# Kernel optimization log

Measured on AMD Instinct MI355X. Metric: run time of the kernel, lower is better.

The kernel has to match this reference:

```python
import jax, jax.numpy as jnp
import numpy as np

N, CAMS = 1, 4
C1, C2, NH = 256, 256, 8
H1, H2, W2 = 128, 64, 400
H, W = 128, 128


def setup_inputs() -> dict:
    key = jax.random.key(0)
    ks = jax.random.split(key, 16)
    sc = 0.02
    th = jax.random.uniform(ks[3], (N, CAMS)) * 2.0 * np.pi
    c, s = jnp.cos(th), jnp.sin(th)
    z, o = jnp.zeros_like(c), jnp.ones_like(c)
    rots = jnp.stack([jnp.stack([c, -s, z], -1), jnp.stack([s, c, z], -1), jnp.stack([z, z, o], -1)], -2)
    return {
        "list_a": jax.random.normal(ks[0], (N, C1, H, W), jnp.float32),
        "list_b": jax.random.normal(ks[1], (N * CAMS, C2, H2, W2), jnp.float32),
        "fov_list": jax.random.uniform(ks[2], (N, CAMS)) * 0.5 + 1.0,
        "rots_list": rots.astype(jnp.float32),
        "trans_list": jax.random.normal(ks[4], (N, CAMS, 3), jnp.float32),
        "fxs": jax.random.uniform(ks[5], (N, CAMS)) * 100.0 + 500.0,
        "cxs": jax.random.uniform(ks[6], (N, CAMS)) * 20.0 + 390.0,
        "pos_a": jax.random.normal(ks[7], (1, H1, C1), jnp.float32),
        "pos_b": jax.random.normal(ks[8], (1, H2, C2), jnp.float32),
        "Wq": jax.random.normal(ks[9], (C1, C1), jnp.float32) * sc,
        "bq": jnp.zeros((C1,), jnp.float32),
        "Wk": jax.random.normal(ks[10], (C1, C2), jnp.float32) * sc,
        "bk": jnp.zeros((C1,), jnp.float32),
        "Wv": jax.random.normal(ks[11], (C1, C2), jnp.float32) * sc,
        "bv": jnp.zeros((C1,), jnp.float32),
        "in_w": jax.random.normal(ks[12], (3 * C1, C1), jnp.float32) * sc,
        "in_b": jnp.zeros((3 * C1,), jnp.float32),
        "out_w": jax.random.normal(ks[13], (C1, C1), jnp.float32) * sc,
        "out_b": jnp.zeros((C1,), jnp.float32),
    }


def _polar_coords(w1, h1, Hh, Ww, rots, fx, cx):
    # per-pixel viewing angles from intrinsics (original image width hard-coded 800)
    pi = jnp.arange(w1, dtype=jnp.float32)
    pw = 800.0 / w1
    ang = jnp.arctan((pi * pw + pw / 2.0 - cx) / fx)
    R90 = jnp.array([[0.0, 1.0], [-1.0, 0.0]], jnp.float32)
    rot = R90 @ rots[:2, :2].astype(jnp.float32)
    cr, sr = rot[0, 0], rot[1, 0]
    ca = cr * jnp.cos(ang) + sr * jnp.sin(ang)
    sa = -sr * jnp.cos(ang) + cr * jnp.sin(ang)
    cxp = jnp.float32(Ww // 2)
    cyp = jnp.float32(Hh // 2)
    rmax = jnp.sqrt(cxp ** 2 + cyp ** 2)
    radii = jnp.linspace(0.0, 1.0, h1).reshape(h1, 1) * rmax
    x = cxp + radii * ca  # [h1, w1]
    y = cyp - radii * sa
    return x, y


def _bilinear(img, x, y):
    # img [C,H,W]; x,y pixel coords [h1,w1]; grid_sample(align_corners=True) after clamping
    Hh, Ww = img.shape[1], img.shape[2]
    x = jnp.clip(x, 0.0, Ww - 1.0)
    y = jnp.clip(y, 0.0, Hh - 1.0)
    x0 = jnp.floor(x); y0 = jnp.floor(y)
    x1 = jnp.clip(x0 + 1.0, 0.0, Ww - 1.0)
    y1 = jnp.clip(y0 + 1.0, 0.0, Hh - 1.0)
    wx = x - x0; wy = y - y0
    x0i, x1i = x0.astype(jnp.int32), x1.astype(jnp.int32)
    y0i, y1i = y0.astype(jnp.int32), y1.astype(jnp.int32)
    v00 = img[:, y0i, x0i]; v01 = img[:, y0i, x1i]
    v10 = img[:, y1i, x0i]; v11 = img[:, y1i, x1i]
    return v00 * (1 - wx) * (1 - wy) + v01 * wx * (1 - wy) + v10 * (1 - wx) * wy + v11 * wx * wy


def _mha(q, k, v, in_w, in_b, out_w, out_b, nh):
    E = q.shape[-1]
    dh = E // nh
    qq = q @ in_w[:E].T + in_b[:E]
    kk = k @ in_w[E:2 * E].T + in_b[E:2 * E]
    vv = v @ in_w[2 * E:].T + in_b[2 * E:]
    B, Lq, _ = q.shape
    Lk = k.shape[1]
    qq = qq.reshape(B, Lq, nh, dh)
    kk = kk.reshape(B, Lk, nh, dh)
    vv = vv.reshape(B, Lk, nh, dh)
    att = jnp.einsum('bqhd,bkhd->bhqk', qq, kk) / jnp.sqrt(jnp.float32(dh))
    p = jax.nn.softmax(att, axis=-1)
    o = jnp.einsum('bhqk,bkhd->bqhd', p, vv).reshape(B, Lq, E)
    return o @ out_w.T + out_b


def _forward(list_a, list_b, rots_list, fxs, cxs, pos_a, pos_b,
             Wq, bq, Wk, bk, Wv, bv, in_w, in_b, out_w, out_b):
    outs = []
    for i in range(list_a.shape[0]):
        a = list_a[i]
        C1_, h1, Wb = a.shape
        Hb = h1
        enh = None
        for j in (0, 3):  # cameras 1 and 2 are skipped by the original `continue`
            b = list_b[i * CAMS + j]
            C2_, h2, w2 = b.shape
            x, y = _polar_coords(w2, h1, a.shape[1], a.shape[2], rots_list[i, j], fxs[i, j], cxs[i, j])
            a_rect = _bilinear(a, x, y)                     # [C1, h1, w2]
            a_seq = jnp.transpose(a_rect, (2, 1, 0)) + pos_a  # [w2, h1, C1]
            b_seq = jnp.transpose(b, (2, 1, 0)) + pos_b       # [w2, h2, C2]
            q = a_seq @ Wq.T + bq
            k = b_seq @ Wk.T + bk
            v = b_seq @ Wv.T + bv
            o = _mha(q, k, v, in_w, in_b, out_w, out_b, NH)
            a_enh = jnp.transpose(o, (2, 1, 0))              # [C1, h1, w2]
            # scatter-add restore with nearest-pixel indices
            xi = jnp.clip(jnp.round(x), 0, a.shape[2] - 1).astype(jnp.int32)
            yi = jnp.clip(jnp.round(y), 0, a.shape[1] - 1).astype(jnp.int32)
            idx = (yi * a.shape[2] + xi).reshape(-1)
            vals = a_enh.reshape(C1_, -1)
            rest = jnp.zeros((C1_, a.shape[1] * a.shape[2]), a.dtype).at[:, idx].add(vals)
            cnt = jnp.zeros((a.shape[1] * a.shape[2],), a.dtype).at[idx].add(1.0)
            cnt = jnp.where(cnt == 0, 1.0, cnt)
            enh = (rest / cnt).reshape(a.shape)
            a = a + enh
        outs.append(a + enh)  # original double-adds the last camera's enhancement
    return jnp.stack(outs)


def reference(list_a, list_b, fov_list, rots_list, trans_list, fxs, cxs, pos_a, pos_b,
              Wq, bq, Wk, bk, Wv, bv, in_w, in_b, out_w, out_b):
    # fov_list / trans_list are accepted but unused in the original math path
    return _forward(list_a, list_b, rots_list, fxs, cxs, pos_a, pos_b,
                    Wq, bq, Wk, bk, Wv, bv, in_w, in_b, out_w, out_b)
```

## Files before the change

### kernel.cpp

```cpp
#include <hip/hip_runtime.h>

#define PIX 16384
#define MS 51200
#define MB 25600

typedef __attribute__((ext_vector_type(8))) short short8;
typedef __attribute__((ext_vector_type(4))) float floatx4;

__device__ inline ushort f2b(float x) {
  uint u = __float_as_uint(x);
  return (ushort)((u + 0x7fffu + ((u >> 16) & 1u)) >> 16);
}
__device__ inline float b2f(ushort u) {
  return __uint_as_float(((uint)u) << 16);
}

__global__ __launch_bounds__(256) void coords_kernel(
    const float* __restrict__ rots, const float* __restrict__ fxs,
    const float* __restrict__ cxs,
    float* __restrict__ xarr, float* __restrict__ yarr,
    int* __restrict__ idxarr, float* __restrict__ cnt)
{
  int jz = blockIdx.y;
  int j = jz ? 3 : 0;
  int s = blockIdx.x * 256 + threadIdx.x;
  int h = s / 400;
  int w = s - h * 400;
  float fx = fxs[j], cx = cxs[j];
  const float* R = rots + j * 9;
  float cr = R[3];
  float sr = -R[0];
  float t = (2.0f * (float)w + 1.0f - cx) / fx;
  float inv = 1.0f / sqrtf(1.0f + t * t);
  float ca = (cr + sr * t) * inv;
  float sa = (cr * t - sr) * inv;
  float rad = ((float)h * (1.0f / 127.0f)) * 90.50966799187808f;
  float x = 64.0f + rad * ca;
  float y = 64.0f - rad * sa;
  xarr[jz * MS + s] = x;
  yarr[jz * MS + s] = y;
  int xi = (int)fminf(fmaxf(rintf(x), 0.0f), 127.0f);
  int yi = (int)fminf(fmaxf(rintf(y), 0.0f), 127.0f);
  int pix = yi * 128 + xi;
  idxarr[jz * MS + s] = pix;
  atomicAdd(&cnt[jz * PIX + pix], 1.0f);
}

__global__ __launch_bounds__(256) void prefix_kernel(
    const float* __restrict__ cntg, int* __restrict__ offsetsg)
{
  const float* cnt = cntg + blockIdx.x * PIX;
  int* offsets = offsetsg + blockIdx.x * PIX;
  __shared__ int sh[256];
  int t = threadIdx.x;
  int base = t * 64;
  const float4* cp = (const float4*)(cnt + base);
  int sum = 0;
#pragma unroll
  for (int i = 0; i < 16; ++i) {
    float4 v = cp[i];
    sum += (int)v.x + (int)v.y + (int)v.z + (int)v.w;
  }
  sh[t] = sum;
  __syncthreads();
  for (int d = 1; d < 256; d <<= 1) {
    int v = (t >= d) ? sh[t - d] : 0;
    __syncthreads();
    sh[t] += v;
    __syncthreads();
  }
  int run = sh[t] - sum;
  int4* op = (int4*)(offsets + base);
#pragma unroll
  for (int i = 0; i < 16; ++i) {
    float4 v = cp[i];
    int a0 = (int)v.x, a1 = (int)v.y, a2 = (int)v.z, a3 = (int)v.w;
    int4 o;
    o.x = run; o.y = run + a0; o.z = run + a0 + a1; o.w = run + a0 + a1 + a2;
    op[i] = o;
    run += a0 + a1 + a2 + a3;
  }
}

__global__ __launch_bounds__(256) void fill_kernel(
    const int* __restrict__ idxarr, const int* __restrict__ offsets,
    int* __restrict__ cursor, int* __restrict__ order, int* __restrict__ pixs)
{
  int jz = blockIdx.y;
  int s = blockIdx.x * 256 + threadIdx.x;
  int pix = idxarr[jz * MS + s];
  int pos = offsets[jz * PIX + pix] + atomicAdd(&cursor[jz * PIX + pix], 1);
  order[jz * MS + pos] = (s % 400) * 128 + (s / 400);
  pixs[jz * MS + pos] = pix;
}

__global__ __launch_bounds__(256) void transpose_kernel(
    const float* __restrict__ src, ushort* __restrict__ dst)
{
  __shared__ float tile[64][65];
  int p0 = blockIdx.x * 64;
  int c0 = blockIdx.y * 64;
  int t = threadIdx.x;
  int pr = (t & 15) * 4;
  int cr = t >> 4;
#pragma unroll
  for (int q = 0; q < 4; ++q) {
    int c = cr + q * 16;
    float4 v = *(const float4*)(src + (size_t)(c0 + c) * PIX + p0 + pr);
    tile[pr + 0][c] = v.x;
    tile[pr + 1][c] = v.y;
    tile[pr + 2][c] = v.z;
    tile[pr + 3][c] = v.w;
  }
  __syncthreads();
  int p = t >> 2;
  int ch = (t & 3) * 16;
  ushort tmp[16];
#pragma unroll
  for (int i = 0; i < 16; ++i) tmp[i] = f2b(tile[p][ch + i]);
  ushort* d = dst + (size_t)(p0 + p) * 256 + c0 + ch;
  *(uint4*)(d) = *(uint4*)tmp;
  *(uint4*)(d + 8) = *(uint4*)(tmp + 8);
}

__global__ __launch_bounds__(256) void misc_kernel(
    const float* __restrict__ out_w, ushort* __restrict__ out_wh,
    const float* __restrict__ in_w, const float* __restrict__ in_b,
    const float* __restrict__ bq, const float* __restrict__ bk,
    const float* __restrict__ bv, float* __restrict__ beff)
{
  if (blockIdx.x < 64) {
    int t = blockIdx.x * 256 + threadIdx.x;
    float4 v = ((const float4*)out_w)[t];
    ushort4 o;
    o.x = f2b(v.x); o.y = f2b(v.y); o.z = f2b(v.z); o.w = f2b(v.w);
    ((ushort4*)out_wh)[t] = o;
  } else {
    int z = blockIdx.x - 64;
    int f = threadIdx.x;
    const float* bsrc = (z == 0) ? bq : ((z == 1) ? bk : bv);
    const float* row = in_w + (size_t)(z * 256 + f) * 256;
    float acc = in_b[z * 256 + f];
    for (int e = 0; e < 256; ++e) acc += row[e] * bsrc[e];
    beff[z * 256 + f] = acc;
  }
}

#define LFP 264
__device__ __forceinline__ void sampleproj_body(
    ushort* lf, int bx,
    const ushort* __restrict__ aT, const float* __restrict__ xarr,
    const float* __restrict__ yarr, const ushort* __restrict__ Wh,
    const float* __restrict__ bias, ushort* __restrict__ qh)
{
  int s0 = bx * 64;
  int tid = threadIdx.x;
  int lane = tid & 63;
  int wave = tid >> 6;
  int col = lane & 15, quad = lane >> 4;
  int c0 = lane * 4;

#pragma unroll 4
  for (int i = 0; i < 16; ++i) {
    int sl = wave * 16 + i;
    int s = s0 + sl;
    float x = fminf(fmaxf(xarr[s], 0.0f), 127.0f);
    float y = fminf(fmaxf(yarr[s], 0.0f), 127.0f);
    float x0f = floorf(x), y0f = floorf(y);
    int x0 = (int)x0f, y0 = (int)y0f;
    int x1 = min(x0 + 1, 127), y1 = min(y0 + 1, 127);
    float wx = x - x0f, wy = y - y0f;
    float w00 = (1.0f - wx) * (1.0f - wy);
    float w01 = wx * (1.0f - wy);
    float w10 = (1.0f - wx) * wy;
    float w11 = wx * wy;
    ushort4 v00 = *(const ushort4*)(aT + (size_t)(y0 * 128 + x0) * 256 + c0);
    ushort4 v01 = *(const ushort4*)(aT + (size_t)(y0 * 128 + x1) * 256 + c0);
    ushort4 v10 = *(const ushort4*)(aT + (size_t)(y1 * 128 + x0) * 256 + c0);
    ushort4 v11 = *(const ushort4*)(aT + (size_t)(y1 * 128 + x1) * 256 + c0);
    ushort4 o;
    o.x = f2b(w00 * b2f(v00.x) + w01 * b2f(v01.x) + w10 * b2f(v10.x) + w11 * b2f(v11.x));
    o.y = f2b(w00 * b2f(v00.y) + w01 * b2f(v01.y) + w10 * b2f(v10.y) + w11 * b2f(v11.y));
    o.z = f2b(w00 * b2f(v00.z) + w01 * b2f(v01.z) + w10 * b2f(v10.z) + w11 * b2f(v11.z));
    o.w = f2b(w00 * b2f(v00.w) + w01 * b2f(v01.w) + w10 * b2f(v10.w) + w11 * b2f(v11.w));
    *(ushort4*)&lf[sl * LFP + c0] = o;
  }
  __syncthreads();

  int fw = wave * 64;
  floatx4 acc[4][4];
#pragma unroll
  for (int i = 0; i < 4; ++i)
#pragma unroll
    for (int jx = 0; jx < 4; ++jx) acc[i][jx] = (floatx4){0.f, 0.f, 0.f, 0.f};

  for (int kb = 0; kb < 256; kb += 32) {
    short8 aop[4], bop[4];
#pragma unroll
    for (int tf = 0; tf < 4; ++tf)
      aop[tf] = *(const short8*)(Wh + (size_t)(fw + tf * 16 + col) * 256 + kb + quad * 8);
#pragma unroll
    for (int ts = 0; ts < 4; ++ts)
      bop[ts] = *(const short8*)&lf[(ts * 16 + col) * LFP + kb + quad * 8];
#pragma unroll
    for (int ts = 0; ts < 4; ++ts)
#pragma unroll
      for (int tf = 0; tf < 4; ++tf)
        acc[ts][tf] = __builtin_amdgcn_mfma_f32_16x16x32_bf16(
            aop[tf], bop[ts], acc[ts][tf], 0, 0, 0);
  }
#pragma unroll
  for (int ts = 0; ts < 4; ++ts) {
    int s = s0 + ts * 16 + col;
    int h = s / 400;
    size_t obase = (size_t)s * 256;
#pragma unroll
    for (int tf = 0; tf < 4; ++tf) {
      int f = fw + tf * 16 + quad * 4;
      float4 bv = *(const float4*)(bias + h * 256 + f);
      ushort4 ov;
      ov.x = f2b(acc[ts][tf][0] + bv.x);
      ov.y = f2b(acc[ts][tf][1] + bv.y);
      ov.z = f2b(acc[ts][tf][2] + bv.z);
      ov.w = f2b(acc[ts][tf][3] + bv.w);
      *(ushort4*)(qh + obase + f) = ov;
    }
  }
}

__device__ __forceinline__ void projKV_body(
    ushort* lb, int bx,
    const float* __restrict__ bsrc,
    const ushort* __restrict__ WhK, const ushort* __restrict__ WhV,
    const float* __restrict__ biasK, const float* __restrict__ biasV,
    ushort* __restrict__ kh, ushort* __restrict__ vh)
{
  int m0 = bx * 64;
  int tid = threadIdx.x;
  int lane = tid & 63;
  int wave = tid >> 6;
  int col = lane & 15, quad = lane >> 4;
  int fw = wave * 64;

  int m4 = (tid & 15) * 4;
  int c4 = (tid >> 4) * 4;
#pragma unroll
  for (int cq = 0; cq < 4; ++cq) {
    int c = c4 + cq * 64;
    float4 v0 = *(const float4*)(bsrc + (size_t)(c + 0) * MB + m0 + m4);
    float4 v1 = *(const float4*)(bsrc + (size_t)(c + 1) * MB + m0 + m4);
    float4 v2 = *(const float4*)(bsrc + (size_t)(c + 2) * MB + m0 + m4);
    float4 v3 = *(const float4*)(bsrc + (size_t)(c + 3) * MB + m0 + m4);
    ushort4 w0; w0.x = f2b(v0.x); w0.y = f2b(v1.x); w0.z = f2b(v2.x); w0.w = f2b(v3.x);
    ushort4 w1; w1.x = f2b(v0.y); w1.y = f2b(v1.y); w1.z = f2b(v2.y); w1.w = f2b(v3.y);
    ushort4 w2; w2.x = f2b(v0.z); w2.y = f2b(v1.z); w2.z = f2b(v2.z); w2.w = f2b(v3.z);
    ushort4 w3; w3.x = f2b(v0.w); w3.y = f2b(v1.w); w3.z = f2b(v2.w); w3.w = f2b(v3.w);
    *(ushort4*)&lb[(m4 + 0) * LFP + c] = w0;
    *(ushort4*)&lb[(m4 + 1) * LFP + c] = w1;
    *(ushort4*)&lb[(m4 + 2) * LFP + c] = w2;
    *(ushort4*)&lb[(m4 + 3) * LFP + c] = w3;
  }
  __syncthreads();

  for (int z = 0; z < 2; ++z) {
    const ushort* Wh = z ? WhV : WhK;
    const float* bias = z ? biasV : biasK;
    ushort* out = z ? vh : kh;
    floatx4 acc[4][4];
#pragma unroll
    for (int i = 0; i < 4; ++i)
#pragma unroll
      for (int jx = 0; jx < 4; ++jx) acc[i][jx] = (floatx4){0.f, 0.f, 0.f, 0.f};

    for (int kb = 0; kb < 256; kb += 32) {
      short8 bop[4], aop[4];
#pragma unroll
      for (int ts = 0; ts < 4; ++ts)
        bop[ts] = *(const short8*)&lb[(ts * 16 + col) * LFP + kb + quad * 8];
#pragma unroll
      for (int tf = 0; tf < 4; ++tf)
        aop[tf] = *(const short8*)(Wh + (size_t)(fw + tf * 16 + col) * 256 + kb + quad * 8);
#pragma unroll
      for (int ts = 0; ts < 4; ++ts)
#pragma unroll
        for (int tf = 0; tf < 4; ++tf)
          acc[ts][tf] = __builtin_amdgcn_mfma_f32_16x16x32_bf16(
              aop[tf], bop[ts], acc[ts][tf], 0, 0, 0);
    }
#pragma unroll
    for (int ts = 0; ts < 4; ++ts) {
      int m = m0 + ts * 16 + col;
      int h = m / 400;
      size_t obase = (size_t)m * 256;
#pragma unroll
      for (int tf = 0; tf < 4; ++tf) {
        int f = fw + tf * 16 + quad * 4;
        float4 bv = *(const float4*)(bias + h * 256 + f);
        ushort4 ov;
        ov.x = f2b(acc[ts][tf][0] + bv.x);
        ov.y = f2b(acc[ts][tf][1] + bv.y);
        ov.z = f2b(acc[ts][tf][2] + bv.z);
        ov.w = f2b(acc[ts][tf][3] + bv.w);
        *(ushort4*)(out + obase + f) = ov;
      }
    }
  }
}

__global__ __launch_bounds__(256, 3) void proj_kernel(
    const ushort* __restrict__ aT, const float* __restrict__ xarr,
    const float* __restrict__ yarr, const ushort* __restrict__ weffh,
    const float* __restrict__ qpos, ushort* __restrict__ qh,
    const float* __restrict__ bsrc,
    const float* __restrict__ kpos, const float* __restrict__ vpos,
    ushort* __restrict__ kh, ushort* __restrict__ vh)
{
  __shared__ ushort lf[64 * LFP];
  if (blockIdx.x < 400)
    projKV_body(lf, blockIdx.x, bsrc, weffh + 65536, weffh + 131072,
                kpos, vpos, kh, vh);
  else
    sampleproj_body(lf, blockIdx.x - 400, aT, xarr, yarr, weffh, qpos, qh);
}

#define VP 72
#define PP 72
__global__ __launch_bounds__(256) void attn_mfma_kernel(
    const ushort* __restrict__ qh, const ushort* __restrict__ kh,
    const ushort* __restrict__ vh, ushort* __restrict__ obuf)
{
  __shared__ ushort lV[4][32 * VP];
  __shared__ ushort lP[4][16 * PP];
  int b = blockIdx.x;
  int hg = blockIdx.y & 1;
  int qb = blockIdx.y >> 1;
  int wave = threadIdx.x >> 6;
  int lane = threadIdx.x & 63;
  int head = hg * 4 + wave;
  int col = lane & 15, quad = lane >> 4;
  ushort* Vw = lV[wave];
  ushort* Pw = lP[wave];

  short8 bk0 = *(const short8*)(kh + ((size_t)(( 0 + col) * 400 + b)) * 256 + head * 32 + quad * 8);
  short8 bk1 = *(const short8*)(kh + ((size_t)((16 + col) * 400 + b)) * 256 + head * 32 + quad * 8);
  short8 bk2 = *(const short8*)(kh + ((size_t)((32 + col) * 400 + b)) * 256 + head * 32 + quad * 8);
  short8 bk3 = *(const short8*)(kh + ((size_t)((48 + col) * 400 + b)) * 256 + head * 32 + quad * 8);

  {
    const ushort* vsrc = vh + ((size_t)(lane * 400 + b)) * 256 + head * 32;
    ushort vr[32];
    *(uint4*)(vr) = *(const uint4*)(vsrc);
    *(uint4*)(vr + 8) = *(const uint4*)(vsrc + 8);
    *(uint4*)(vr + 16) = *(const uint4*)(vsrc + 16);
    *(uint4*)(vr + 24) = *(const uint4*)(vsrc + 24);
#pragma unroll
    for (int d = 0; d < 32; ++d) Vw[d * VP + lane] = vr[d];
  }
  short8 vA0 = *(const short8*)(Vw + (col) * VP + 0 * 32 + quad * 8);
  short8 vB0 = *(const short8*)(Vw + (16 + col) * VP + 0 * 32 + quad * 8);
  short8 vA1 = *(const short8*)(Vw + (col) * VP + 1 * 32 + quad * 8);
  short8 vB1 = *(const short8*)(Vw + (16 + col) * VP + 1 * 32 + quad * 8);

  const float scl = 0.17677669529663687f;
  for (int qt = qb * 4; qt < qb * 4 + 4; ++qt) {
    short8 aq = *(const short8*)(qh +
        ((size_t)((qt * 16 + col) * 400 + b)) * 256 + head * 32 + quad * 8);
    floatx4 s0 = {0.f,0.f,0.f,0.f}, s1 = s0, s2 = s0, s3 = s0;
    s0 = __builtin_amdgcn_mfma_f32_16x16x32_bf16(aq, bk0, s0, 0, 0, 0);
    s1 = __builtin_amdgcn_mfma_f32_16x16x32_bf16(aq, bk1, s1, 0, 0, 0);
    s2 = __builtin_amdgcn_mfma_f32_16x16x32_bf16(aq, bk2, s2, 0, 0, 0);
    s3 = __builtin_amdgcn_mfma_f32_16x16x32_bf16(aq, bk3, s3, 0, 0, 0);
    float e[4][4], mr[4], sm[4];
#pragma unroll
    for (int r = 0; r < 4; ++r) {
      float v0 = s0[r] * scl, v1 = s1[r] * scl;
      float v2 = s2[r] * scl, v3 = s3[r] * scl;
      e[0][r] = v0; e[1][r] = v1; e[2][r] = v2; e[3][r] = v3;
      mr[r] = fmaxf(fmaxf(v0, v1), fmaxf(v2, v3));
    }
#pragma unroll
    for (int mask = 1; mask <= 8; mask <<= 1)
#pragma unroll
      for (int r = 0; r < 4; ++r)
        mr[r] = fmaxf(mr[r], __shfl_xor(mr[r], mask, 64));
#pragma unroll
    for (int r = 0; r < 4; ++r) {
      float acc = 0.f;
#pragma unroll
      for (int t = 0; t < 4; ++t) {
        float ev = __expf(e[t][r] - mr[r]);
        e[t][r] = ev;
        acc += ev;
      }
      sm[r] = acc;
    }
#pragma unroll
    for (int mask = 1; mask <= 8; mask <<= 1)
#pragma unroll
      for (int r = 0; r < 4; ++r)
        sm[r] += __shfl_xor(sm[r], mask, 64);
#pragma unroll
    for (int t = 0; t < 4; ++t)
#pragma unroll
      for (int r = 0; r < 4; ++r)
        Pw[(quad * 4 + r) * PP + t * 16 + col] = f2b(e[t][r]);
    floatx4 o0 = {0.f,0.f,0.f,0.f}, o1 = o0;
    {
      short8 ap0 = *(const short8*)(Pw + col * PP + 0 * 32 + quad * 8);
      o0 = __builtin_amdgcn_mfma_f32_16x16x32_bf16(ap0, vA0, o0, 0, 0, 0);
      o1 = __builtin_amdgcn_mfma_f32_16x16x32_bf16(ap0, vB0, o1, 0, 0, 0);
      short8 ap1 = *(const short8*)(Pw + col * PP + 1 * 32 + quad * 8);
      o0 = __builtin_amdgcn_mfma_f32_16x16x32_bf16(ap1, vA1, o0, 0, 0, 0);
      o1 = __builtin_amdgcn_mfma_f32_16x16x32_bf16(ap1, vB1, o1, 0, 0, 0);
    }
#pragma unroll
    for (int r = 0; r < 4; ++r) {
      float iv = 1.0f / sm[r];
      Pw[(quad * 4 + r) * PP + col] = f2b(o0[r] * iv);
      Pw[(quad * 4 + r) * PP + 16 + col] = f2b(o1[r] * iv);
    }
    int orow = lane >> 2, ochunk = lane & 3;
    uint4 ov = *(const uint4*)(Pw + orow * PP + ochunk * 8);
    *(uint4*)(obuf + (size_t)(b * 128 + qt * 16 + orow) * 256 + head * 32 + ochunk * 8) = ov;
  }
}

__global__ __launch_bounds__(256) void gemmN3_kernel(
    const float* __restrict__ pos_a, const float* __restrict__ pos_b,
    const float* __restrict__ weff, const float* __restrict__ beff,
    float* __restrict__ qpos, float* __restrict__ kpos, float* __restrict__ vpos)
{
  int z = blockIdx.z;
  if (z > 0 && blockIdx.x > 0) return;
  const float* A = (z == 0) ? pos_a : pos_b;
  const float* Wt = weff + (size_t)z * 65536;
  const float* biasf = beff + z * 256;
  float* Cout = (z == 0) ? qpos : ((z == 1) ? kpos : vpos);
  __shared__ float As[64][17];
  __shared__ float Ws[16][65];
  int m0 = blockIdx.x * 64;
  int n0 = blockIdx.y * 64;
  int tid = threadIdx.x;
  int tx = tid & 15, ty = tid >> 4;
  float acc[4][4] = {};
  for (int k0 = 0; k0 < 256; k0 += 16) {
    {
      int m = tid >> 2;
      int kq = (tid & 3) << 2;
      float4 v = *(const float4*)(A + (size_t)(m0 + m) * 256 + k0 + kq);
      As[m][kq + 0] = v.x; As[m][kq + 1] = v.y;
      As[m][kq + 2] = v.z; As[m][kq + 3] = v.w;
    }
    {
      int f = tid >> 2;
      int kq = (tid & 3) << 2;
      float4 v = *(const float4*)(Wt + (size_t)(n0 + f) * 256 + k0 + kq);
      Ws[kq + 0][f] = v.x; Ws[kq + 1][f] = v.y;
      Ws[kq + 2][f] = v.z; Ws[kq + 3][f] = v.w;
    }
    __syncthreads();
#pragma unroll
    for (int kk = 0; kk < 16; ++kk) {
      float a[4], b[4];
#pragma unroll
      for (int i = 0; i < 4; ++i) a[i] = As[ty * 4 + i][kk];
#pragma unroll
      for (int jj = 0; jj < 4; ++jj) b[jj] = Ws[kk][tx * 4 + jj];
#pragma unroll
      for (int i = 0; i < 4; ++i)
#pragma unroll
        for (int jj = 0; jj < 4; ++jj) acc[i][jj] += a[i] * b[jj];
    }
    __syncthreads();
  }
#pragma unroll
  for (int i = 0; i < 4; ++i) {
    int m = m0 + ty * 4 + i;
    int f = n0 + tx * 4;
    float4 bv = *(const float4*)(biasf + f);
    float4 ov;
    ov.x = acc[i][0] + bv.x; ov.y = acc[i][1] + bv.y;
    ov.z = acc[i][2] + bv.z; ov.w = acc[i][3] + bv.w;
    *(float4*)(Cout + (size_t)m * 256 + f) = ov;
  }
}

__global__ __launch_bounds__(256) void gemm_ab_kernel(
    const float* __restrict__ in_w, const float* __restrict__ Wq,
    const float* __restrict__ Wk, const float* __restrict__ Wv,
    float* __restrict__ weff, ushort* __restrict__ weffh)
{
  int z = blockIdx.z;
  const float* A = in_w + (size_t)z * 65536;
  const float* B = (z == 0) ? Wq : ((z == 1) ? Wk : Wv);
  float* C = weff + (size_t)z * 65536;
  ushort* Ch = weffh + (size_t)z * 65536;
  __shared__ float As[64][17];
  __shared__ float Bs[16][64];
  int m0 = blockIdx.x * 64;
  int n0 = blockIdx.y * 64;
  int tid = threadIdx.x;
  int tx = tid & 15, ty = tid >> 4;
  float acc[4][4] = {};
  for (int k0 = 0; k0 < 256; k0 += 16) {
    {
      int m = tid >> 2;
      int kq = (tid & 3) << 2;
      float4 v = *(const float4*)(A + (size_t)(m0 + m) * 256 + k0 + kq);
      As[m][kq + 0] = v.x; As[m][kq + 1] = v.y;
      As[m][kq + 2] = v.z; As[m][kq + 3] = v.w;
    }
    {
      int k = tid >> 4;
      int nq = (tid & 15) << 2;
      float4 v = *(const float4*)(B + (size_t)(k0 + k) * 256 + n0 + nq);
      *(float4*)(&Bs[k][nq]) = v;
    }
    __syncthreads();
#pragma unroll
    for (int kk = 0; kk < 16; ++kk) {
      float a[4], b[4];
#pragma unroll
      for (int i = 0; i < 4; ++i) a[i] = As[ty * 4 + i][kk];
#pragma unroll
      for (int jj = 0; jj < 4; ++jj) b[jj] = Bs[kk][tx * 4 + jj];
#pragma unroll
      for (int i = 0; i < 4; ++i)
#pragma unroll
        for (int jj = 0; jj < 4; ++jj) acc[i][jj] += a[i] * b[jj];
    }
    __syncthreads();
  }
#pragma unroll
  for (int i = 0; i < 4; ++i) {
    int m = m0 + ty * 4 + i;
    *(float4*)(C + (size_t)m * 256 + n0 + tx * 4) = *(float4*)&acc[i][0];
    ushort4 hv;
    hv.x = f2b(acc[i][0]); hv.y = f2b(acc[i][1]);
    hv.z = f2b(acc[i][2]); hv.w = f2b(acc[i][3]);
    *(ushort4*)(Ch + (size_t)m * 256 + n0 + tx * 4) = hv;
  }
}

#define CH 64
__global__ __launch_bounds__(256) void segred_kernel(
    const ushort* __restrict__ obuf, const int* __restrict__ order,
    const int* __restrict__ pixs, float* __restrict__ osum)
{
  __shared__ int lm[CH];
  __shared__ int lp[CH + 2];
  int s0 = blockIdx.x * CH;
  int t = threadIdx.x;
  if (t < CH) {
    lm[t] = order[s0 + t];
    lp[t + 1] = pixs[s0 + t];
  } else if (t == CH) {
    lp[0] = (s0 > 0) ? pixs[s0 - 1] : -1;
  } else if (t == CH + 1) {
    lp[CH + 1] = (s0 + CH < MS) ? pixs[s0 + CH] : -2;
  }
  __syncthreads();
  int c = t;
  float va[8];
#pragma unroll
  for (int k = 0; k < 8; ++k)
    va[k] = b2f(obuf[(size_t)lm[k] * 256 + c]);
  float acc = 0.0f;
  int runBegin = 0;
#pragma unroll
  for (int i = 0; i < CH; ++i) {
    float v = va[i & 7];
    if (i + 8 < CH) va[i & 7] = b2f(obuf[(size_t)lm[i + 8] * 256 + c]);
    acc += v;
    int p = lp[i + 1];
    bool last = (i == CH - 1);
    if (last || p != lp[i + 2]) {
      bool pBeg = (runBegin == 0) && (p == lp[0]);
      bool pEnd = last && (p == lp[CH + 1]);
      float* dst = osum + (size_t)p * 256 + c;
      if (pBeg || pEnd) atomicAdd(dst, acc);
      else *dst = acc;
      acc = 0.0f;
      runBegin = i + 1;
    }
  }
}

__global__ __launch_bounds__(256) void outproj_update_kernel(
    const float* __restrict__ osum, const ushort* __restrict__ out_wh,
    const float* __restrict__ asrc, float* __restrict__ adst,
    const float* __restrict__ cnt, const float* __restrict__ out_b,
    float scale, ushort* __restrict__ aTout, int writeAT)
{
  int p0 = blockIdx.x * 32;
  int lane = threadIdx.x & 63;
  int wave = threadIdx.x >> 6;
  int col = lane & 15, quad = lane >> 4;
  int fw = wave * 64;
  floatx4 acc[2][4];
#pragma unroll
  for (int i = 0; i < 2; ++i)
#pragma unroll
    for (int jx = 0; jx < 4; ++jx) acc[i][jx] = (floatx4){0.f, 0.f, 0.f, 0.f};

  for (int kb = 0; kb < 256; kb += 32) {
    short8 aop[4], bop[2];
#pragma unroll
    for (int tf = 0; tf < 4; ++tf)
      aop[tf] = *(const short8*)(out_wh +
          (size_t)(fw + tf * 16 + col) * 256 + kb + quad * 8);
#pragma unroll
    for (int ts = 0; ts < 2; ++ts) {
      const float* brow = osum + (size_t)(p0 + ts * 16 + col) * 256 + kb + quad * 8;
      float4 f0 = *(const float4*)brow;
      float4 f1 = *(const float4*)(brow + 4);
      short8 bv;
      bv[0] = (short)f2b(f0.x); bv[1] = (short)f2b(f0.y);
      bv[2] = (short)f2b(f0.z); bv[3] = (short)f2b(f0.w);
      bv[4] = (short)f2b(f1.x); bv[5] = (short)f2b(f1.y);
      bv[6] = (short)f2b(f1.z); bv[7] = (short)f2b(f1.w);
      bop[ts] = bv;
    }
#pragma unroll
    for (int ts = 0; ts < 2; ++ts)
#pragma unroll
      for (int tf = 0; tf < 4; ++tf)
        acc[ts][tf] = __builtin_amdgcn_mfma_f32_16x16x32_bf16(
            aop[tf], bop[ts], acc[ts][tf], 0, 0, 0);
  }
#pragma unroll
  for (int ts = 0; ts < 2; ++ts) {
    int p = p0 + ts * 16 + col;
    float cn = cnt[p];
    float rs = scale / fmaxf(cn, 1.0f);
#pragma unroll
    for (int tf = 0; tf < 4; ++tf) {
      int f = fw + tf * 16 + quad * 4;
      float4 ob = *(const float4*)(out_b + f);
      float r0 = asrc[(size_t)(f + 0) * PIX + p] + (acc[ts][tf][0] + cn * ob.x) * rs;
      float r1 = asrc[(size_t)(f + 1) * PIX + p] + (acc[ts][tf][1] + cn * ob.y) * rs;
      float r2 = asrc[(size_t)(f + 2) * PIX + p] + (acc[ts][tf][2] + cn * ob.z) * rs;
      float r3 = asrc[(size_t)(f + 3) * PIX + p] + (acc[ts][tf][3] + cn * ob.w) * rs;
      adst[(size_t)(f + 0) * PIX + p] = r0;
      adst[(size_t)(f + 1) * PIX + p] = r1;
      adst[(size_t)(f + 2) * PIX + p] = r2;
      adst[(size_t)(f + 3) * PIX + p] = r3;
      if (writeAT) {
        ushort4 hv;
        hv.x = f2b(r0); hv.y = f2b(r1); hv.z = f2b(r2); hv.w = f2b(r3);
        *(ushort4*)(aTout + (size_t)p * 256 + f) = hv;
      }
    }
  }
}

extern "C" void kernel_launch(void* const* d_in, const int* in_sizes, int n_in,
                              void* d_out, int out_size, void* d_ws, size_t ws_size,
                              hipStream_t stream) {
  const float* list_a = (const float*)d_in[0];
  const float* list_b = (const float*)d_in[1];
  const float* rots   = (const float*)d_in[3];
  const float* fxs    = (const float*)d_in[5];
  const float* cxs    = (const float*)d_in[6];
  const float* pos_a  = (const float*)d_in[7];
  const float* pos_b  = (const float*)d_in[8];
  const float* Wq     = (const float*)d_in[9];
  const float* bq     = (const float*)d_in[10];
  const float* Wk     = (const float*)d_in[11];
  const float* bk     = (const float*)d_in[12];
  const float* Wv     = (const float*)d_in[13];
  const float* bv     = (const float*)d_in[14];
  const float* in_w   = (const float*)d_in[15];
  const float* in_b   = (const float*)d_in[16];
  const float* out_w  = (const float*)d_in[17];
  const float* out_b  = (const float*)d_in[18];

  float* ws      = (float*)d_ws;
  float* weff    = ws;
  float* beff    = weff + 196608;
  float* qpos    = beff + 768;
  float* kpos    = qpos + 32768;
  float* vpos    = kpos + 16384;
  float* a_cur   = vpos + 16384;
  float* xarr    = a_cur + 4194304;
  float* yarr    = xarr + 102400;
  int*   idxarr  = (int*)(yarr + 102400);
  int*   offs    = idxarr + 102400;
  int*   order   = offs + 32768;
  int*   pixs    = order + 102400;
  float* cnt     = (float*)(pixs + 102400);
  int*   cursor  = (int*)(cnt + 32768);
  float* osum    = (float*)(cursor + 32768);
  ushort* weffh  = (ushort*)(osum + 4194304);
  ushort* out_wh = weffh + 196608;
  ushort* obufh  = out_wh + 65536;
  ushort* qh     = obufh + 13107200;
  ushort* kh     = qh + 13107200;
  ushort* vh     = kh + 6553600;
  ushort* aT     = vh + 6553600;

  gemm_ab_kernel<<<dim3(4, 4, 3), 256, 0, stream>>>(in_w, Wq, Wk, Wv, weff, weffh);
  misc_kernel<<<67, 256, 0, stream>>>(out_w, out_wh, in_w, in_b, bq, bk, bv, beff);
  gemmN3_kernel<<<dim3(2, 4, 3), 256, 0, stream>>>(pos_a, pos_b, weff, beff,
                                                   qpos, kpos, vpos);
  hipMemsetAsync(cnt, 0, (size_t)(32768 + 32768) * sizeof(float), stream);
  coords_kernel<<<dim3(200, 2), 256, 0, stream>>>(rots, fxs, cxs, xarr, yarr, idxarr, cnt);
  prefix_kernel<<<2, 256, 0, stream>>>(cnt, offs);
  fill_kernel<<<dim3(200, 2), 256, 0, stream>>>(idxarr, offs, cursor, order, pixs);

  for (int jj = 0; jj < 2; ++jj) {
    int j = jj ? 3 : 0;
    const float* asrc = jj ? a_cur : list_a;
    hipMemsetAsync(osum, 0, (size_t)4194304 * sizeof(float), stream);
    if (jj == 0)
      transpose_kernel<<<dim3(256, 4), 256, 0, stream>>>(list_a, aT);
    proj_kernel<<<1200, 256, 0, stream>>>(aT, xarr + jj * MS, yarr + jj * MS,
                                          weffh, qpos, qh,
                                          list_b + (size_t)j * 6553600,
                                          kpos, vpos, kh, vh);
    attn_mfma_kernel<<<dim3(400, 4), 256, 0, stream>>>(qh, kh, vh, obufh);
    segred_kernel<<<800, 256, 0, stream>>>(obufh, order + jj * MS, pixs + jj * MS, osum);
    outproj_update_kernel<<<512, 256, 0, stream>>>(osum, out_wh, asrc,
                                                   jj ? (float*)d_out : a_cur,
                                                   cnt + jj * PIX, out_b,
                                                   jj ? 2.0f : 1.0f,
                                                   aT, jj == 0 ? 1 : 0);
  }
}
```

Measured before the change: 549.5 us.

## Fuse segmented reduction into out-projection kernel via CSR gather into LDS

Replaces the segment-reduce kernel, which wrote per-pixel sums to a global fp32 buffer with atomics, and the separate out-projection kernel with one kernel. The new kernel gathers each pixel's samples through the CSR offsets and counts, sums them into shared memory, and runs the MFMA out-projection from LDS. This drops the 16 MB osum memset, the global write and re-read of osum, and one launch per camera. The per-pixel gather loops vary in length, so work across waves may be uneven. Separately, proj_kernel's launch bounds move from 3 to 4 waves per EU, which may increase register pressure.

```diff
diff --git a/kernel.cpp b/kernel.cpp
--- a/kernel.cpp
+++ b/kernel.cpp
@@ -307,7 +307,7 @@
   }
 }
 
-__global__ __launch_bounds__(256, 3) void proj_kernel(
+__global__ __launch_bounds__(256, 4) void proj_kernel(
     const ushort* __restrict__ aT, const float* __restrict__ xarr,
     const float* __restrict__ yarr, const ushort* __restrict__ weffh,
     const float* __restrict__ qpos, ushort* __restrict__ qh,
@@ -542,59 +542,40 @@
   }
 }
 
-#define CH 64
-__global__ __launch_bounds__(256) void segred_kernel(
+#define OLF 260
+__global__ __launch_bounds__(256) void outred_kernel(
     const ushort* __restrict__ obuf, const int* __restrict__ order,
-    const int* __restrict__ pixs, float* __restrict__ osum)
-{
-  __shared__ int lm[CH];
-  __shared__ int lp[CH + 2];
-  int s0 = blockIdx.x * CH;
-  int t = threadIdx.x;
-  if (t < CH) {
-    lm[t] = order[s0 + t];
-    lp[t + 1] = pixs[s0 + t];
-  } else if (t == CH) {
-    lp[0] = (s0 > 0) ? pixs[s0 - 1] : -1;
-  } else if (t == CH + 1) {
-    lp[CH + 1] = (s0 + CH < MS) ? pixs[s0 + CH] : -2;
+    const int* __restrict__ offs, const float* __restrict__ cnt,
+    const ushort* __restrict__ out_wh,
+    const float* __restrict__ asrc, float* __restrict__ adst,
+    const float* __restrict__ out_b, float scale,
+    ushort* __restrict__ aTout, int writeAT)
+{
+  __shared__ float losum[32 * OLF];
+  int p0 = blockIdx.x * 32;
+  int tid = threadIdx.x;
+
+  {
+    int pg = tid >> 6;
+    int c0 = (tid & 63) * 4;
+    for (int pi = 0; pi < 8; ++pi) {
+      int p = p0 + pg * 8 + pi;
+      int beg = offs[p];
+      int num = (int)cnt[p];
+      float4 s4 = {0.f, 0.f, 0.f, 0.f};
+      for (int i = 0; i < num; ++i) {
+        int m = order[beg + i];
+        ushort4 v = *(const ushort4*)(obuf + (size_t)m * 256 + c0);
+        s4.x += b2f(v.x); s4.y += b2f(v.y);
+        s4.z += b2f(v.z); s4.w += b2f(v.w);
+      }
+      *(float4*)&losum[(pg * 8 + pi) * OLF + c0] = s4;
+    }
   }
   __syncthreads();
-  int c = t;
-  float va[8];
-#pragma unroll
-  for (int k = 0; k < 8; ++k)
-    va[k] = b2f(obuf[(size_t)lm[k] * 256 + c]);
-  float acc = 0.0f;
-  int runBegin = 0;
-#pragma unroll
-  for (int i = 0; i < CH; ++i) {
-    float v = va[i & 7];
-    if (i + 8 < CH) va[i & 7] = b2f(obuf[(size_t)lm[i + 8] * 256 + c]);
-    acc += v;
-    int p = lp[i + 1];
-    bool last = (i == CH - 1);
-    if (last || p != lp[i + 2]) {
-      bool pBeg = (runBegin == 0) && (p == lp[0]);
-      bool pEnd = last && (p == lp[CH + 1]);
-      float* dst = osum + (size_t)p * 256 + c;
-      if (pBeg || pEnd) atomicAdd(dst, acc);
-      else *dst = acc;
-      acc = 0.0f;
-      runBegin = i + 1;
-    }
-  }
-}
-
-__global__ __launch_bounds__(256) void outproj_update_kernel(
-    const float* __restrict__ osum, const ushort* __restrict__ out_wh,
-    const float* __restrict__ asrc, float* __restrict__ adst,
-    const float* __restrict__ cnt, const float* __restrict__ out_b,
-    float scale, ushort* __restrict__ aTout, int writeAT)
-{
-  int p0 = blockIdx.x * 32;
-  int lane = threadIdx.x & 63;
-  int wave = threadIdx.x >> 6;
+
+  int lane = tid & 63;
+  int wave = tid >> 6;
   int col = lane & 15, quad = lane >> 4;
   int fw = wave * 64;
   floatx4 acc[2][4];
@@ -611,7 +592,7 @@
           (size_t)(fw + tf * 16 + col) * 256 + kb + quad * 8);
 #pragma unroll
     for (int ts = 0; ts < 2; ++ts) {
-      const float* brow = osum + (size_t)(p0 + ts * 16 + col) * 256 + kb + quad * 8;
+      const float* brow = &losum[(ts * 16 + col) * OLF + kb + quad * 8];
       float4 f0 = *(const float4*)brow;
       float4 f1 = *(const float4*)(brow + 4);
       short8 bv;
@@ -690,8 +671,7 @@
   int*   pixs    = order + 102400;
   float* cnt     = (float*)(pixs + 102400);
   int*   cursor  = (int*)(cnt + 32768);
-  float* osum    = (float*)(cursor + 32768);
-  ushort* weffh  = (ushort*)(osum + 4194304);
+  ushort* weffh  = (ushort*)(cursor + 32768);
   ushort* out_wh = weffh + 196608;
   ushort* obufh  = out_wh + 65536;
   ushort* qh     = obufh + 13107200;
@@ -711,7 +691,6 @@
   for (int jj = 0; jj < 2; ++jj) {
     int j = jj ? 3 : 0;
     const float* asrc = jj ? a_cur : list_a;
-    hipMemsetAsync(osum, 0, (size_t)4194304 * sizeof(float), stream);
     if (jj == 0)
       transpose_kernel<<<dim3(256, 4), 256, 0, stream>>>(list_a, aT);
     proj_kernel<<<1200, 256, 0, stream>>>(aT, xarr + jj * MS, yarr + jj * MS,
@@ -719,11 +698,11 @@
                                           list_b + (size_t)j * 6553600,
                                           kpos, vpos, kh, vh);
     attn_mfma_kernel<<<dim3(400, 4), 256, 0, stream>>>(qh, kh, vh, obufh);
-    segred_kernel<<<800, 256, 0, stream>>>(obufh, order + jj * MS, pixs + jj * MS, osum);
-    outproj_update_kernel<<<512, 256, 0, stream>>>(osum, out_wh, asrc,
-                                                   jj ? (float*)d_out : a_cur,
-                                                   cnt + jj * PIX, out_b,
-                                                   jj ? 2.0f : 1.0f,
-                                                   aT, jj == 0 ? 1 : 0);
-  }
-}
+    outred_kernel<<<512, 256, 0, stream>>>(obufh, order + jj * MS,
+                                           offs + jj * PIX, cnt + jj * PIX,
+                                           out_wh, asrc,
+                                           jj ? (float*)d_out : a_cur,
+                                           out_b, jj ? 2.0f : 1.0f,
+                                           aT, jj == 0 ? 1 : 0);
+  }
+}
```

After: 1.626 ms. 196% more time.
